# Kernel tuning notes

Hardware: AMD Instinct MI355X
Metric: run time of the kernel (lower is better)

## Reference

```python
import jax, jax.numpy as jnp
import numpy as np

T, B, E, H = 512, 32, 512, 2048

def setup_inputs() -> dict:
    key = jax.random.key(0)
    k1, k2, k3 = jax.random.split(key, 3)
    sent = jax.random.normal(k1, (T, B, E), dtype=jnp.float32)
    lengths = jax.random.randint(k2, (B,), 1, T + 1)  # unused by the math (pack is never applied)
    # Linear(E, 3H) params (PyTorch default-ish init scale)
    W = jax.random.normal(k3, (3 * H, E), dtype=jnp.float32) * (1.0 / np.sqrt(E))
    b = jnp.zeros((3 * H,), dtype=jnp.float32)
    return {"sent": sent, "lengths": lengths, "W": W, "b": b}

def reference(sent, lengths, W, b):
    # sent: (T, B, E) time-major. Single QRNN layer, window=1, output_gate=True, zoneout=0.
    Y = jnp.einsum('tbe,he->tbh', sent, W) + b          # (T, B, 3H)
    Z, F, O = jnp.split(Y, 3, axis=-1)
    Z = jnp.tanh(Z)
    F = jax.nn.sigmoid(F)
    O = jax.nn.sigmoid(O)

    # forget-mult recurrence: c_t = f_t * z_t + (1 - f_t) * c_{t-1}, c_0 = 0
    def step(c, zf):
        z, f = zf
        c = f * z + (1.0 - f) * c
        return c, c
    c0 = jnp.zeros_like(Z[0])                            # (B, H)
    _, C = jax.lax.scan(step, c0, (Z, F))                # (T, B, H)

    Hseq = O * C                                         # QRNN output (T, B, H)
    embeds = jnp.max(Hseq, axis=0)                       # torch.max(sent_output, 0)[0] -> (B, H)
    return embeds
```

## Files before the change

### kernel.cpp

```cpp
#include <hip/hip_runtime.h>
#include <stdint.h>

#define TT 512
#define BB 32
#define EE 512
#define HH 2048

typedef __attribute__((ext_vector_type(8))) short short8;
typedef __attribute__((ext_vector_type(4))) float f32x4;

#define XROW 528
#define XBUF (16 * XROW)

static __device__ __forceinline__ float fast_exp(float x) {
    return __builtin_amdgcn_exp2f(x * 1.44269504f);
}
static __device__ __forceinline__ float fast_rcp(float x) {
    return __builtin_amdgcn_rcpf(x);
}

static __device__ __forceinline__ unsigned cvtpk_bf16(float lo, float hi) {
    unsigned r;
    asm("v_cvt_pk_bf16_f32 %0, %1, %2" : "=v"(r) : "v"(lo), "v"(hi));
    return r;
}

static __device__ __forceinline__ void load_lds16(const unsigned short* g, unsigned short* l) {
    __builtin_amdgcn_global_load_lds(
        (const __attribute__((address_space(1))) unsigned int*)(uintptr_t)g,
        (__attribute__((address_space(3))) unsigned int*)(uintptr_t)l,
        16, 0, 0);
}

__launch_bounds__(256, 8)
__global__ void convert_inputs(const float* __restrict__ X,
                               const float* __restrict__ W,
                               unsigned short* __restrict__ Xb,
                               unsigned short* __restrict__ Wb) {
    const int bid = blockIdx.x;
    const float* src;
    unsigned short* dst;
    size_t base;
    if (bid < 2048) { src = X; dst = Xb; base = (size_t)bid * 4096; }
    else            { src = W; dst = Wb; base = (size_t)(bid - 2048) * 4096; }
    size_t j = base + (size_t)threadIdx.x * 16;

    float4 v0 = *(const float4*)(src + j);
    float4 v1 = *(const float4*)(src + j + 4);
    float4 v2 = *(const float4*)(src + j + 8);
    float4 v3 = *(const float4*)(src + j + 12);
    union { short8 s; unsigned u[4]; } o0, o1;
    o0.u[0] = cvtpk_bf16(v0.x, v0.y);
    o0.u[1] = cvtpk_bf16(v0.z, v0.w);
    o0.u[2] = cvtpk_bf16(v1.x, v1.y);
    o0.u[3] = cvtpk_bf16(v1.z, v1.w);
    o1.u[0] = cvtpk_bf16(v2.x, v2.y);
    o1.u[1] = cvtpk_bf16(v2.z, v2.w);
    o1.u[2] = cvtpk_bf16(v3.x, v3.y);
    o1.u[3] = cvtpk_bf16(v3.z, v3.w);
    *(short8*)(dst + j)     = o0.s;
    *(short8*)(dst + j + 8) = o1.s;
}

__launch_bounds__(256, 2)
__global__ void qrnn_fused(const unsigned short* __restrict__ Xb,
                           const unsigned short* __restrict__ Wb,
                           const float* __restrict__ bias,
                           float* __restrict__ out)
{
    __shared__ unsigned short xlds[2 * XBUF];
    __shared__ float exch[2][2][64][12];

    const int tid  = threadIdx.x;
    const int wv   = tid >> 6;
    const int lane = tid & 63;
    const int q    = lane >> 4;
    const int c    = lane & 15;
    const int hi   = wv >> 1;
    const int s    = wv & 1;

    const int id   = blockIdx.x;
    const int xcd  = id & 7;
    const int slot = id >> 3;
    const int b    = xcd * 4 + (slot >> 6);
    const int hgrp = slot & 63;
    const int h    = hgrp * 32 + hi * 16 + c;

    short8 wz[8], wf[8], wo[8];
    {
        const unsigned short* wzr = Wb + (size_t)h * EE            + s * 256;
        const unsigned short* wfr = Wb + (size_t)(HH + h) * EE     + s * 256;
        const unsigned short* wor = Wb + (size_t)(2 * HH + h) * EE + s * 256;
#pragma unroll
        for (int k = 0; k < 8; ++k) {
            int e0 = k * 32 + q * 8;
            wz[k] = *(const short8*)(wzr + e0);
            wf[k] = *(const short8*)(wfr + e0);
            wo[k] = *(const short8*)(wor + e0);
        }
    }
#pragma unroll
    for (int k = 0; k < 8; ++k) {
        asm volatile("" : "+a"(wz[k]), "+a"(wf[k]), "+a"(wo[k]));
    }

    const float b0 = (s == 0) ? bias[h]          : 0.0f;
    const float b1 = (s == 0) ? bias[HH + h]     : 0.0f;
    const float b2 = (s == 0) ? bias[2 * HH + h] : 0.0f;

    float carry = 0.0f;
    float vmax  = -1e30f;

    const unsigned short* g0 = Xb + ((size_t)(wv * 4) * BB + b) * EE + lane * 8;
    unsigned short* l0 = &xlds[(wv * 4) * XROW];

    auto stage = [&](int n, int slt) {
        const unsigned short* g = g0 + (size_t)n * (16 * BB * EE);
        unsigned short* l = l0 + slt * XBUF;
#pragma unroll
        for (int i = 0; i < 4; ++i)
            load_lds16(g + (size_t)i * (BB * EE), l + i * XROW);
    };

    auto do_tail = [&](f32x4 az, f32x4 af, f32x4 ao) {
        float aa[4], mm[4], oo[4];
#pragma unroll
        for (int r = 0; r < 4; ++r) {
            float e2 = fast_exp(2.0f * az[r]);
            float z  = 1.0f - 2.0f * fast_rcp(e2 + 1.0f);
            float f  = fast_rcp(1.0f + fast_exp(-af[r]));
            float o  = fast_rcp(1.0f + fast_exp(-ao[r]));
            aa[r] = f * z;
            mm[r] = 1.0f - f;
            oo[r] = o;
        }

        float A = aa[0], M = mm[0];
#pragma unroll
        for (int r = 1; r < 4; ++r) { A = aa[r] + mm[r] * A; M = mm[r] * M; }

        float Ap = __shfl_up(A, 16, 64), Mp = __shfl_up(M, 16, 64);
        if (q >= 1) { A = A + M * Ap; M = M * Mp; }
        Ap = __shfl_up(A, 32, 64); Mp = __shfl_up(M, 32, 64);
        if (q >= 2) { A = A + M * Ap; M = M * Mp; }
        float Ae = __shfl_up(A, 16, 64), Me = __shfl_up(M, 16, 64);
        if (q == 0) { Ae = 0.0f; Me = 1.0f; }
        float cc = Ae + Me * carry;

#pragma unroll
        for (int r = 0; r < 4; ++r) {
            cc = aa[r] + mm[r] * cc;
            vmax = fmaxf(vmax, oo[r] * cc);
        }

        float cend = A + M * carry;
        carry = __shfl(cend, 48 + c, 64);
    };

    stage(0, 0);
    __syncthreads();

    f32x4 prevz, prevf, prevo;

    for (int ch = 0; ch < 32; ++ch) {
        const int buf = ch & 1;
        if (ch < 31) stage(ch + 1, buf ^ 1);

        const unsigned short* Abase = &xlds[buf * XBUF + c * XROW + s * 256 + q * 8];
        short8 a[8];
#pragma unroll
        for (int k = 0; k < 8; ++k)
            a[k] = *(const short8*)(Abase + k * 32);

        f32x4 pz, pf, po;
        if (s == 0 && ch > 0) {
            const float* e = &exch[(ch - 1) & 1][hi][lane][0];
            pz = *(const f32x4*)(e);
            pf = *(const f32x4*)(e + 4);
            po = *(const f32x4*)(e + 8);
        }

        f32x4 az = {b0, b0, b0, b0};
        f32x4 af = {b1, b1, b1, b1};
        f32x4 ao = {b2, b2, b2, b2};
        __builtin_amdgcn_s_setprio(1);
#pragma unroll
        for (int k = 0; k < 8; ++k) {
            az = __builtin_amdgcn_mfma_f32_16x16x32_bf16(a[k], wz[k], az, 0, 0, 0);
            af = __builtin_amdgcn_mfma_f32_16x16x32_bf16(a[k], wf[k], af, 0, 0, 0);
            ao = __builtin_amdgcn_mfma_f32_16x16x32_bf16(a[k], wo[k], ao, 0, 0, 0);
        }
        __builtin_amdgcn_s_setprio(0);

        if (s == 1) {
            float* e = &exch[ch & 1][hi][lane][0];
            *(f32x4*)(e)     = az;
            *(f32x4*)(e + 4) = af;
            *(f32x4*)(e + 8) = ao;
        }

        if (s == 0 && ch > 0) {
            do_tail(prevz + pz, prevf + pf, prevo + po);
        }

        prevz = az; prevf = af; prevo = ao;

        __syncthreads();
    }

    if (s == 0) {
        const float* e = &exch[31 & 1][hi][lane][0];
        f32x4 pz = *(const f32x4*)(e);
        f32x4 pf = *(const f32x4*)(e + 4);
        f32x4 po = *(const f32x4*)(e + 8);
        do_tail(prevz + pz, prevf + pf, prevo + po);

        vmax = fmaxf(vmax, __shfl_xor(vmax, 16, 64));
        vmax = fmaxf(vmax, __shfl_xor(vmax, 32, 64));
        if (q == 0) out[(size_t)b * HH + h] = vmax;
    }
}

extern "C" void kernel_launch(void* const* d_in, const int* in_sizes, int n_in,
                              void* d_out, int out_size, void* d_ws, size_t ws_size,
                              hipStream_t stream) {
    const float* sent = (const float*)d_in[0];
    const float* W    = (const float*)d_in[2];
    const float* bias = (const float*)d_in[3];
    float* out        = (float*)d_out;

    const int nX = TT * BB * EE;
    unsigned short* Xb = (unsigned short*)d_ws;
    unsigned short* Wb = Xb + nX;

    convert_inputs<<<2816, 256, 0, stream>>>(sent, W, Xb, Wb);

    dim3 grid(2048);
    qrnn_fused<<<grid, 256, 0, stream>>>(Xb, Wb, bias, out);
}
```

Baseline: 234.7 us.

## Specialize warps into three gate-GEMM warps and one dedicated scan warp

```diff
diff --git a/kernel.cpp b/kernel.cpp
--- a/kernel.cpp
+++ b/kernel.cpp
@@ -62,54 +62,50 @@
     *(short8*)(dst + j + 8) = o1.s;
 }
 
-__launch_bounds__(256, 2)
+__launch_bounds__(256, 3)
 __global__ void qrnn_fused(const unsigned short* __restrict__ Xb,
                            const unsigned short* __restrict__ Wb,
                            const float* __restrict__ bias,
                            float* __restrict__ out)
 {
     __shared__ unsigned short xlds[2 * XBUF];
-    __shared__ float exch[2][2][64][12];
+    __shared__ float exch[2][64][12];
 
     const int tid  = threadIdx.x;
     const int wv   = tid >> 6;
     const int lane = tid & 63;
     const int q    = lane >> 4;
     const int c    = lane & 15;
-    const int hi   = wv >> 1;
-    const int s    = wv & 1;
 
     const int id   = blockIdx.x;
     const int xcd  = id & 7;
     const int slot = id >> 3;
-    const int b    = xcd * 4 + (slot >> 6);
-    const int hgrp = slot & 63;
-    const int h    = hgrp * 32 + hi * 16 + c;
-
-    short8 wz[8], wf[8], wo[8];
-    {
-        const unsigned short* wzr = Wb + (size_t)h * EE            + s * 256;
-        const unsigned short* wfr = Wb + (size_t)(HH + h) * EE     + s * 256;
-        const unsigned short* wor = Wb + (size_t)(2 * HH + h) * EE + s * 256;
-#pragma unroll
-        for (int k = 0; k < 8; ++k) {
-            int e0 = k * 32 + q * 8;
-            wz[k] = *(const short8*)(wzr + e0);
-            wf[k] = *(const short8*)(wfr + e0);
-            wo[k] = *(const short8*)(wor + e0);
-        }
-    }
-#pragma unroll
-    for (int k = 0; k < 8; ++k) {
-        asm volatile("" : "+a"(wz[k]), "+a"(wf[k]), "+a"(wo[k]));
-    }
-
-    const float b0 = (s == 0) ? bias[h]          : 0.0f;
-    const float b1 = (s == 0) ? bias[HH + h]     : 0.0f;
-    const float b2 = (s == 0) ? bias[2 * HH + h] : 0.0f;
+    const int b    = xcd * 4 + (slot >> 7);
+    const int hgrp = slot & 127;
+    const int h    = hgrp * 16 + c;
+
+    const int  scanwv = slot & 3;
+    const bool isScan = (wv == scanwv);
+    const int  gsel   = (wv < scanwv) ? wv : wv - 1;
 
     float carry = 0.0f;
     float vmax  = -1e30f;
+    float b0 = 0.f, b1 = 0.f, b2 = 0.f;
+
+    short8 wg[16];
+    if (!isScan) {
+        const unsigned short* wr = Wb + ((size_t)gsel * HH + h) * EE;
+#pragma unroll
+        for (int k = 0; k < 16; ++k)
+            wg[k] = *(const short8*)(wr + k * 32 + q * 8);
+#pragma unroll
+        for (int k = 0; k < 16; ++k)
+            asm volatile("" : "+a"(wg[k]));
+    } else {
+        b0 = bias[h];
+        b1 = bias[HH + h];
+        b2 = bias[2 * HH + h];
+    }
 
     const unsigned short* g0 = Xb + ((size_t)(wv * 4) * BB + b) * EE + lane * 8;
     unsigned short* l0 = &xlds[(wv * 4) * XROW];
@@ -160,60 +156,53 @@
     stage(0, 0);
     __syncthreads();
 
-    f32x4 prevz, prevf, prevo;
-
     for (int ch = 0; ch < 32; ++ch) {
         const int buf = ch & 1;
         if (ch < 31) stage(ch + 1, buf ^ 1);
 
-        const unsigned short* Abase = &xlds[buf * XBUF + c * XROW + s * 256 + q * 8];
-        short8 a[8];
-#pragma unroll
-        for (int k = 0; k < 8; ++k)
-            a[k] = *(const short8*)(Abase + k * 32);
-
-        f32x4 pz, pf, po;
-        if (s == 0 && ch > 0) {
-            const float* e = &exch[(ch - 1) & 1][hi][lane][0];
-            pz = *(const f32x4*)(e);
-            pf = *(const f32x4*)(e + 4);
-            po = *(const f32x4*)(e + 8);
+        if (!isScan) {
+            const unsigned short* Abase = &xlds[buf * XBUF + c * XROW + q * 8];
+            f32x4 ac0 = {0.f, 0.f, 0.f, 0.f};
+            f32x4 ac1 = {0.f, 0.f, 0.f, 0.f};
+#pragma unroll
+            for (int half = 0; half < 2; ++half) {
+                short8 a[8];
+#pragma unroll
+                for (int j = 0; j < 8; ++j)
+                    a[j] = *(const short8*)(Abase + (half * 8 + j) * 32);
+#pragma unroll
+                for (int j = 0; j < 8; ++j) {
+                    if (j & 1)
+                        ac1 = __builtin_amdgcn_mfma_f32_16x16x32_bf16(a[j], wg[half * 8 + j], ac1, 0, 0, 0);
+                    else
+                        ac0 = __builtin_amdgcn_mfma_f32_16x16x32_bf16(a[j], wg[half * 8 + j], ac0, 0, 0, 0);
+                }
+            }
+            f32x4 ac = ac0 + ac1;
+            *(f32x4*)(&exch[ch & 1][lane][gsel * 4]) = ac;
+        } else {
+            if (ch > 0) {
+                const float* e = &exch[(ch - 1) & 1][lane][0];
+                f32x4 az = *(const f32x4*)(e);
+                f32x4 af = *(const f32x4*)(e + 4);
+                f32x4 ao = *(const f32x4*)(e + 8);
+#pragma unroll
+                for (int r = 0; r < 4; ++r) { az[r] += b0; af[r] += b1; ao[r] += b2; }
+                do_tail(az, af, ao);
+            }
         }
-
-        f32x4 az = {b0, b0, b0, b0};
-        f32x4 af = {b1, b1, b1, b1};
-        f32x4 ao = {b2, b2, b2, b2};
-        __builtin_amdgcn_s_setprio(1);
-#pragma unroll
-        for (int k = 0; k < 8; ++k) {
-            az = __builtin_amdgcn_mfma_f32_16x16x32_bf16(a[k], wz[k], az, 0, 0, 0);
-            af = __builtin_amdgcn_mfma_f32_16x16x32_bf16(a[k], wf[k], af, 0, 0, 0);
-            ao = __builtin_amdgcn_mfma_f32_16x16x32_bf16(a[k], wo[k], ao, 0, 0, 0);
-        }
-        __builtin_amdgcn_s_setprio(0);
-
-        if (s == 1) {
-            float* e = &exch[ch & 1][hi][lane][0];
-            *(f32x4*)(e)     = az;
-            *(f32x4*)(e + 4) = af;
-            *(f32x4*)(e + 8) = ao;
-        }
-
-        if (s == 0 && ch > 0) {
-            do_tail(prevz + pz, prevf + pf, prevo + po);
-        }
-
-        prevz = az; prevf = af; prevo = ao;
 
         __syncthreads();
     }
 
-    if (s == 0) {
-        const float* e = &exch[31 & 1][hi][lane][0];
-        f32x4 pz = *(const f32x4*)(e);
-        f32x4 pf = *(const f32x4*)(e + 4);
-        f32x4 po = *(const f32x4*)(e + 8);
-        do_tail(prevz + pz, prevf + pf, prevo + po);
+    if (isScan) {
+        const float* e = &exch[31 & 1][lane][0];
+        f32x4 az = *(const f32x4*)(e);
+        f32x4 af = *(const f32x4*)(e + 4);
+        f32x4 ao = *(const f32x4*)(e + 8);
+#pragma unroll
+        for (int r = 0; r < 4; ++r) { az[r] += b0; af[r] += b1; ao[r] += b2; }
+        do_tail(az, af, ao);
 
         vmax = fmaxf(vmax, __shfl_xor(vmax, 16, 64));
         vmax = fmaxf(vmax, __shfl_xor(vmax, 32, 64));
@@ -235,6 +224,6 @@
 
     convert_inputs<<<2816, 256, 0, stream>>>(sent, W, Xb, Wb);
 
-    dim3 grid(2048);
+    dim3 grid(4096);
     qrnn_fused<<<grid, 256, 0, stream>>>(Xb, Wb, bias, out);
 }
```

Result: no change. 237.8 us (+1.3%).
